# Kernel tuning notes

Measured on AMD Instinct MI355X. Metric: run time of the kernel, lower is better.

The kernel has to match this reference:

```python
import jax, jax.numpy as jnp
import numpy as np


def setup_inputs() -> dict:
    key = jax.random.key(0)
    ks = jax.random.split(key, 8)
    B, L, C = 128, 196, 2048  # batch, locations (att_size^2), channels
    H, D = 512, 1024          # att_hid_size, decoder hidden_size
    return {
        "att_features": jax.random.normal(ks[0], (B, L, C), dtype=jnp.float32),
        "h": jax.random.normal(ks[1], (B, D), dtype=jnp.float32),
        "Wc": jax.random.normal(ks[2], (L, H), dtype=jnp.float32) * 0.05,
        "bc": jax.random.normal(ks[3], (H,), dtype=jnp.float32) * 0.05,
        "Wh": jax.random.normal(ks[4], (D, H), dtype=jnp.float32) * 0.05,
        "bh": jax.random.normal(ks[5], (H,), dtype=jnp.float32) * 0.05,
        "wa": jax.random.normal(ks[6], (H,), dtype=jnp.float32) * 0.05,
        "ba": jnp.zeros((1,), dtype=jnp.float32),
    }


def reference(att_features, h, Wc, bc, Wh, bh, wa, ba):
    B, L, C = att_features.shape
    # reshape to (B, locations, C) then permute -> (B, C, locations)
    x = jnp.transpose(att_features.reshape(B, L, C), (0, 2, 1))  # (B, C, L)
    ca = jnp.einsum('bcl,lh->bch', x, Wc) + bc                   # channel2att: (B, C, H)
    ph = h @ Wh + bh                                              # h2att: (B, H)
    # alpha_net(tanh(broadcast add)) -> (B, C)
    scores = jnp.einsum('bch,h->bc', jnp.tanh(ca + ph[:, None, :]), wa) + ba[0]
    weights = jax.nn.softmax(scores, axis=1)                      # softmax over channels
    # bmm: (B,1,C) @ (B,C,L) -> (B, L)
    weighted = jnp.einsum('bc,bcl->bl', weights, x)
    return weighted, weights
```

## Files before the change

### kernel.cpp

```cpp
#include <hip/hip_runtime.h>

#define B_   128
#define L_   196
#define C_   2048
#define H_   512
#define D_   1024
#define KP   224
#define ALD  232
#define CT   128
#define HM   128
#define NITER 28

typedef __bf16 bf16x8 __attribute__((ext_vector_type(8)));
typedef __bf16 bf16x4 __attribute__((ext_vector_type(4)));
typedef float  f32x4  __attribute__((ext_vector_type(4)));

__global__ __launch_bounds__(256) void k_wc(const float* __restrict__ Wc, __bf16* __restrict__ wcb) {
    int tid = blockIdx.x * 256 + threadIdx.x;
    int hh = tid / KP;
    int k  = tid - hh * KP;
    float v = (k < L_) ? Wc[(size_t)k * H_ + hh] : 0.0f;
    wcb[tid] = (__bf16)v;
}

__global__ __launch_bounds__(512) void k_ph(const float* __restrict__ h, const float* __restrict__ Wh,
                                            const float* __restrict__ bh, const float* __restrict__ bc,
                                            float* __restrict__ ph_ws) {
    int b0 = blockIdx.x * 4;
    int t = threadIdx.x;
    __shared__ float hs[4][D_];
    for (int idx = t; idx < 4 * D_; idx += 512)
        hs[idx >> 10][idx & (D_ - 1)] = h[(size_t)(b0 + (idx >> 10)) * D_ + (idx & (D_ - 1))];
    __syncthreads();
    float base = bh[t] + bc[t];
    float a0 = base, a1 = base, a2 = base, a3 = base;
#pragma unroll 8
    for (int d = 0; d < D_; ++d) {
        float wv = Wh[(size_t)d * H_ + t];
        a0 += hs[0][d] * wv; a1 += hs[1][d] * wv; a2 += hs[2][d] * wv; a3 += hs[3][d] * wv;
    }
    ph_ws[(size_t)(b0 + 0) * H_ + t] = a0;
    ph_ws[(size_t)(b0 + 1) * H_ + t] = a1;
    ph_ws[(size_t)(b0 + 2) * H_ + t] = a2;
    ph_ws[(size_t)(b0 + 3) * H_ + t] = a3;
}

__device__ __forceinline__ float fast_tanh(float x) {
    x = fminf(fmaxf(x, -15.f), 15.f);
    float e = __builtin_amdgcn_exp2f(x * 2.8853900817779268f);
    return 1.0f - 2.0f * __builtin_amdgcn_rcpf(e + 1.0f);
}

__device__ __forceinline__ void stage_wc(const __bf16* __restrict__ wcb, __bf16* dst,
                                         int hc, int kk, int wid, int lane) {
#pragma unroll
    for (int jj = 0; jj < 2; ++jj) {
        int i = wid * 2 + jj;
        const __bf16* g = wcb + (size_t)(hc * HM + i * 16 + (lane >> 2)) * KP + kk * 32 + (lane & 3) * 8;
        __bf16* lp = dst + i * 512;
        __builtin_amdgcn_global_load_lds((__attribute__((address_space(1))) void*)g,
                                         (__attribute__((address_space(3))) void*)lp, 16, 0, 0);
    }
}

__global__ __launch_bounds__(256) void k_scores(const float* __restrict__ att, const __bf16* __restrict__ wcb,
                                                const float* __restrict__ ph_ws, const float* __restrict__ wa,
                                                const float* __restrict__ ba, float* __restrict__ scores) {
    __shared__ __bf16 att_s[CT * ALD];
    __shared__ __bf16 wc_s[2][HM * 32];
    __shared__ float  sred[2][2][4][16];

    const int t = threadIdx.x;
    const int lane = t & 63, wid = t >> 6;
    const int wm = wid >> 1, wn = wid & 1;
    const int ct = blockIdx.x, b = blockIdx.y;

    stage_wc(wcb, &wc_s[0][0], 0, 0, wid, lane);

    {
        const __bf16 z = (__bf16)0.0f;
        bf16x4 z4 = {z, z, z, z};
        for (int idx = t; idx < CT * 7; idx += 256) {
            int c = idx / 7, kq = idx - (idx / 7) * 7;
            *(bf16x4*)&att_s[c * ALD + L_ + kq * 4] = z4;
        }
    }
    {
        const float* abase = att + ((size_t)b * L_) * C_ + ct * CT;
        for (int task = t; task < (CT / 4) * (L_ / 4); task += 256) {
            int cq = task & 31;
            int lq = task >> 5;
            const float* ap = abase + (size_t)(lq * 4) * C_ + cq * 4;
            f32x4 r0 = *(const f32x4*)(ap);
            f32x4 r1 = *(const f32x4*)(ap + C_);
            f32x4 r2 = *(const f32x4*)(ap + 2 * C_);
            f32x4 r3 = *(const f32x4*)(ap + 3 * C_);
#pragma unroll
            for (int i2 = 0; i2 < 4; ++i2) {
                bf16x4 v = {(__bf16)r0[i2], (__bf16)r1[i2], (__bf16)r2[i2], (__bf16)r3[i2]};
                *(bf16x4*)&att_s[(cq * 4 + i2) * ALD + lq * 4] = v;
            }
        }
    }
    __syncthreads();

    const int aoff = (wm * 64 + (lane & 15)) * 32 + (lane >> 4) * 8;
    const int boff = (wn * 64 + (lane & 15)) * ALD + (lane >> 4) * 8;

    f32x4 zero4 = {0.f, 0.f, 0.f, 0.f};
    f32x4 acc[4][4];
#pragma unroll
    for (int mf = 0; mf < 4; ++mf)
#pragma unroll
        for (int nf = 0; nf < 4; ++nf) acc[mf][nf] = zero4;
    float spart[4] = {0.f, 0.f, 0.f, 0.f};

    for (int i = 0; i < NITER; ++i) {
        const int hc = i / 7;
        const int kk = i - hc * 7;
        const int buf = i & 1;
        if (i + 1 < NITER) {
            const int i2 = i + 1;
            stage_wc(wcb, &wc_s[buf ^ 1][0], i2 / 7, i2 - (i2 / 7) * 7, wid, lane);
        }
        bf16x8 afr[4], bfr[4];
#pragma unroll
        for (int mf = 0; mf < 4; ++mf) afr[mf] = *(const bf16x8*)&wc_s[buf][aoff + mf * 512];
#pragma unroll
        for (int nf = 0; nf < 4; ++nf) bfr[nf] = *(const bf16x8*)&att_s[boff + nf * 16 * ALD + kk * 32];
#pragma unroll
        for (int mf = 0; mf < 4; ++mf)
#pragma unroll
            for (int nf = 0; nf < 4; ++nf)
                acc[mf][nf] = __builtin_amdgcn_mfma_f32_16x16x32_bf16(afr[mf], bfr[nf], acc[mf][nf], 0, 0, 0);

        if (kk == 6) {
            const int rbase = hc * HM + wm * 64 + (lane >> 4) * 4;
#pragma unroll
            for (int mf = 0; mf < 4; ++mf) {
                const int row = rbase + mf * 16;
                f32x4 phv = *(const f32x4*)&ph_ws[(size_t)b * H_ + row];
                f32x4 wav = *(const f32x4*)&wa[row];
#pragma unroll
                for (int nf = 0; nf < 4; ++nf) {
                    f32x4 tv = acc[mf][nf];
                    float ssum = 0.f;
#pragma unroll
                    for (int r = 0; r < 4; ++r) {
                        float x = tv[r] + phv[r];
                        ssum += fast_tanh(x) * wav[r];
                    }
                    spart[nf] += ssum;
                    acc[mf][nf] = zero4;
                }
            }
        }
        __syncthreads();
    }

#pragma unroll
    for (int nf = 0; nf < 4; ++nf) {
        spart[nf] += __shfl_xor(spart[nf], 16);
        spart[nf] += __shfl_xor(spart[nf], 32);
    }
    if ((lane >> 4) == 0) {
#pragma unroll
        for (int nf = 0; nf < 4; ++nf) sred[wm][wn][nf][lane] = spart[nf];
    }
    __syncthreads();
    if (wm == 0 && (lane >> 4) == 0) {
        const float ba0 = ba[0];
#pragma unroll
        for (int nf = 0; nf < 4; ++nf) {
            float v = sred[0][wn][nf][lane] + sred[1][wn][nf][lane] + ba0;
            scores[(size_t)b * C_ + ct * CT + wn * 64 + nf * 16 + lane] = v;
        }
    }
}

__global__ __launch_bounds__(256) void k_softmax(const float* __restrict__ sc, float* __restrict__ wout) {
    int b = blockIdx.x, t = threadIdx.x;
    int lane = t & 63, wid = t >> 6;
    const float* sp = sc + (size_t)b * C_;
    float v[8];
#pragma unroll
    for (int j = 0; j < 8; ++j) v[j] = sp[j * 256 + t];
    float m = v[0];
#pragma unroll
    for (int j = 1; j < 8; ++j) m = fmaxf(m, v[j]);
#pragma unroll
    for (int off = 32; off >= 1; off >>= 1) m = fmaxf(m, __shfl_xor(m, off));
    __shared__ float red[4];
    if (lane == 0) red[wid] = m;
    __syncthreads();
    m = fmaxf(fmaxf(red[0], red[1]), fmaxf(red[2], red[3]));
    float s = 0.f;
#pragma unroll
    for (int j = 0; j < 8; ++j) {
        v[j] = __builtin_amdgcn_exp2f((v[j] - m) * 1.4426950408889634f);
        s += v[j];
    }
#pragma unroll
    for (int off = 32; off >= 1; off >>= 1) s += __shfl_xor(s, off);
    __shared__ float red2[4];
    if (lane == 0) red2[wid] = s;
    __syncthreads();
    s = red2[0] + red2[1] + red2[2] + red2[3];
    float inv = __builtin_amdgcn_rcpf(s);
#pragma unroll
    for (int j = 0; j < 8; ++j) wout[(size_t)b * C_ + j * 256 + t] = v[j] * inv;
}

__global__ __launch_bounds__(256) void k_weighted(const float* __restrict__ att, const float* __restrict__ w,
                                                  float* __restrict__ out) {
    int b = blockIdx.y;
    int wid = threadIdx.x >> 6, lane = threadIdx.x & 63;
    int l = blockIdx.x * 4 + wid;
    const float* ap = att + ((size_t)b * L_ + l) * C_;
    const float* wp = w + (size_t)b * C_;
    float acc = 0.f;
#pragma unroll
    for (int j = 0; j < 8; ++j) {
        int c = j * 256 + lane * 4;
        f32x4 a4 = *(const f32x4*)(ap + c);
        f32x4 w4 = *(const f32x4*)(wp + c);
        acc += a4[0] * w4[0] + a4[1] * w4[1] + a4[2] * w4[2] + a4[3] * w4[3];
    }
#pragma unroll
    for (int off = 32; off >= 1; off >>= 1) acc += __shfl_xor(acc, off);
    if (lane == 0) out[(size_t)b * L_ + l] = acc;
}

extern "C" void kernel_launch(void* const* d_in, const int* in_sizes, int n_in,
                              void* d_out, int out_size, void* d_ws, size_t ws_size,
                              hipStream_t stream) {
    const float* att = (const float*)d_in[0];
    const float* h   = (const float*)d_in[1];
    const float* Wc  = (const float*)d_in[2];
    const float* bc  = (const float*)d_in[3];
    const float* Wh  = (const float*)d_in[4];
    const float* bh  = (const float*)d_in[5];
    const float* wa  = (const float*)d_in[6];
    const float* ba  = (const float*)d_in[7];
    float* out = (float*)d_out;

    float* ph_ws  = (float*)d_ws;
    float* scores = ph_ws + B_ * H_;
    __bf16* wcb   = (__bf16*)(scores + (size_t)B_ * C_);

    k_wc      <<<dim3((H_ * KP) / 256), 256, 0, stream>>>(Wc, wcb);
    k_ph      <<<dim3(B_ / 4), 512, 0, stream>>>(h, Wh, bh, bc, ph_ws);
    k_scores  <<<dim3(C_ / CT, B_), 256, 0, stream>>>(att, wcb, ph_ws, wa, ba, scores);
    k_softmax <<<dim3(B_), 256, 0, stream>>>(scores, out + B_ * L_);
    k_weighted<<<dim3(L_ / 4, B_), 256, 0, stream>>>(att, out + B_ * L_, out);
}
```

Measured before the change: 481.8 us.

## Rework scores GEMM tiling with swizzled LDS, register-held Wc, and fuse softmax+weighted

The scores kernel moves to 512-thread blocks covering 256 channels with the whole attention tile staged in a swizzled LDS layout. Staging is now pipelined with the MFMA loop, so the input copy overlaps compute and the per-iteration barriers after staging are dropped. Wc is pre-packed into MFMA fragment order and loaded straight from global memory into registers with prefetch, replacing the LDS double buffer. Softmax and the weighted sum are fused into one kernel that keeps the weights in shared memory. The price is higher register and LDS use per block (128KB dynamic LDS, 32 accumulators per lane), which may limit occupancy, plus softmax being recomputed in 4 blocks per batch.

```diff
diff --git a/kernel.cpp b/kernel.cpp
--- a/kernel.cpp
+++ b/kernel.cpp
@@ -6,21 +6,31 @@
 #define H_   512
 #define D_   1024
 #define KP   224
-#define ALD  232
-#define CT   128
-#define HM   128
-#define NITER 28
+#define CT   256
+#define NITER 14
+
+#define SMEM_BYTES (131072 + 4096)
 
 typedef __bf16 bf16x8 __attribute__((ext_vector_type(8)));
-typedef __bf16 bf16x4 __attribute__((ext_vector_type(4)));
+typedef float  f32x2  __attribute__((ext_vector_type(2)));
 typedef float  f32x4  __attribute__((ext_vector_type(4)));
 
-__global__ __launch_bounds__(256) void k_wc(const float* __restrict__ Wc, __bf16* __restrict__ wcb) {
-    int tid = blockIdx.x * 256 + threadIdx.x;
-    int hh = tid / KP;
-    int k  = tid - hh * KP;
-    float v = (k < L_) ? Wc[(size_t)k * H_ + hh] : 0.0f;
-    wcb[tid] = (__bf16)v;
+__device__ __forceinline__ int permc(int c) { return ((c >> 2) & 7) ^ ((c & 2) << 1); }
+
+__global__ __launch_bounds__(256) void k_wc3(const float* __restrict__ Wc, __bf16* __restrict__ wcb3) {
+    int grp = blockIdx.x * 256 + threadIdx.x;
+    int m  = grp & 15;
+    int g  = (grp >> 4) & 3;
+    int rb = (grp >> 6) & 31;
+    int kk = grp >> 11;
+    int h  = rb * 16 + m;
+    bf16x8 v;
+#pragma unroll
+    for (int j = 0; j < 8; ++j) {
+        int k = kk * 32 + g * 8 + j;
+        v[j] = (k < L_) ? (__bf16)Wc[(size_t)k * H_ + h] : (__bf16)0.0f;
+    }
+    *(bf16x8*)&wcb3[(size_t)grp * 8] = v;
 }
 
 __global__ __launch_bounds__(512) void k_ph(const float* __restrict__ h, const float* __restrict__ Wh,
@@ -51,184 +61,199 @@
     return 1.0f - 2.0f * __builtin_amdgcn_rcpf(e + 1.0f);
 }
 
-__device__ __forceinline__ void stage_wc(const __bf16* __restrict__ wcb, __bf16* dst,
-                                         int hc, int kk, int wid, int lane) {
-#pragma unroll
-    for (int jj = 0; jj < 2; ++jj) {
-        int i = wid * 2 + jj;
-        const __bf16* g = wcb + (size_t)(hc * HM + i * 16 + (lane >> 2)) * KP + kk * 32 + (lane & 3) * 8;
-        __bf16* lp = dst + i * 512;
-        __builtin_amdgcn_global_load_lds((__attribute__((address_space(1))) void*)g,
-                                         (__attribute__((address_space(3))) void*)lp, 16, 0, 0);
-    }
-}
-
-__global__ __launch_bounds__(256) void k_scores(const float* __restrict__ att, const __bf16* __restrict__ wcb,
-                                                const float* __restrict__ ph_ws, const float* __restrict__ wa,
-                                                const float* __restrict__ ba, float* __restrict__ scores) {
-    __shared__ __bf16 att_s[CT * ALD];
-    __shared__ __bf16 wc_s[2][HM * 32];
-    __shared__ float  sred[2][2][4][16];
-
-    const int t = threadIdx.x;
-    const int lane = t & 63, wid = t >> 6;
+__global__ __launch_bounds__(512, 2) void k_scores(const float* __restrict__ att, const __bf16* __restrict__ wcb3,
+                                                   const float* __restrict__ ph_ws, const float* __restrict__ wa,
+                                                   const float* __restrict__ ba, float* __restrict__ scores) {
+    extern __shared__ char smem[];
+    __bf16* att_s = (__bf16*)smem;
+    float*  sred  = (float*)(smem + 131072);
+
+    const int t = threadIdx.x, lane = t & 63, wid = t >> 6;
     const int wm = wid >> 1, wn = wid & 1;
     const int ct = blockIdx.x, b = blockIdx.y;
-
-    stage_wc(wcb, &wc_s[0][0], 0, 0, wid, lane);
-
-    {
-        const __bf16 z = (__bf16)0.0f;
-        bf16x4 z4 = {z, z, z, z};
-        for (int idx = t; idx < CT * 7; idx += 256) {
-            int c = idx / 7, kq = idx - (idx / 7) * 7;
-            *(bf16x4*)&att_s[c * ALD + L_ + kq * 4] = z4;
-        }
-    }
-    {
-        const float* abase = att + ((size_t)b * L_) * C_ + ct * CT;
-        for (int task = t; task < (CT / 4) * (L_ / 4); task += 256) {
-            int cq = task & 31;
-            int lq = task >> 5;
-            const float* ap = abase + (size_t)(lq * 4) * C_ + cq * 4;
-            f32x4 r0 = *(const f32x4*)(ap);
-            f32x4 r1 = *(const f32x4*)(ap + C_);
-            f32x4 r2 = *(const f32x4*)(ap + 2 * C_);
-            f32x4 r3 = *(const f32x4*)(ap + 3 * C_);
-#pragma unroll
-            for (int i2 = 0; i2 < 4; ++i2) {
-                bf16x4 v = {(__bf16)r0[i2], (__bf16)r1[i2], (__bf16)r2[i2], (__bf16)r3[i2]};
-                *(bf16x4*)&att_s[(cq * 4 + i2) * ALD + lq * 4] = v;
-            }
-        }
-    }
-    __syncthreads();
-
-    const int aoff = (wm * 64 + (lane & 15)) * 32 + (lane >> 4) * 8;
-    const int boff = (wn * 64 + (lane & 15)) * ALD + (lane >> 4) * 8;
+    const float* attb = att + ((size_t)b * L_) * C_ + ct * CT;
+
+    const int cpr = t & 127, sl = t >> 7;
+    const int c0s = cpr * 2;
+    const int pmS = permc(c0s);
+
+    const int n_ = lane & 15, g_ = lane >> 4;
+    const int crow0 = wn * 128 + n_;
+    const int t2 = (n_ & 2) << 1;
+    const int qb = crow0 >> 2;
+
+    f32x2 sv[8];
+    auto STAGE_LOAD = [&](int kk) {
+#pragma unroll
+        for (int j = 0; j < 8; ++j) {
+            int l = kk * 32 + sl * 8 + j;
+            if (l < L_) sv[j] = *(const f32x2*)(attb + (size_t)l * C_ + c0s);
+            else { sv[j][0] = 0.f; sv[j][1] = 0.f; }
+        }
+    };
+    auto STAGE_WRITE = [&](int kk) {
+        int p = (kk * 4 + sl) ^ pmS;
+        bf16x8 r0, r1;
+#pragma unroll
+        for (int j = 0; j < 8; ++j) { r0[j] = (__bf16)sv[j][0]; r1[j] = (__bf16)sv[j][1]; }
+        *(bf16x8*)&att_s[c0s * 256 + p * 8] = r0;
+        *(bf16x8*)&att_s[(c0s + 1) * 256 + p * 8] = r1;
+    };
+
+    bf16x8 afr[4], afrN[4];
+    const __bf16* apA = wcb3 + (size_t)lane * 8;
+    auto ALOAD = [&](int it, bf16x8* dst) {
+        int hc = (it >= 7) ? 1 : 0;
+        int kk = it - hc * 7;
+#pragma unroll
+        for (int mf = 0; mf < 4; ++mf) {
+            int rb = hc * 16 + wm * 4 + mf;
+            dst[mf] = *(const bf16x8*)(apA + (size_t)(kk * 32 + rb) * 512);
+        }
+    };
+
+    ALOAD(0, afr);
+    STAGE_LOAD(0);
+    STAGE_WRITE(0);
+    __syncthreads();
 
     f32x4 zero4 = {0.f, 0.f, 0.f, 0.f};
-    f32x4 acc[4][4];
+    f32x4 acc[4][8];
 #pragma unroll
     for (int mf = 0; mf < 4; ++mf)
 #pragma unroll
-        for (int nf = 0; nf < 4; ++nf) acc[mf][nf] = zero4;
-    float spart[4] = {0.f, 0.f, 0.f, 0.f};
-
-    for (int i = 0; i < NITER; ++i) {
-        const int hc = i / 7;
-        const int kk = i - hc * 7;
-        const int buf = i & 1;
-        if (i + 1 < NITER) {
-            const int i2 = i + 1;
-            stage_wc(wcb, &wc_s[buf ^ 1][0], i2 / 7, i2 - (i2 / 7) * 7, wid, lane);
-        }
-        bf16x8 afr[4], bfr[4];
-#pragma unroll
-        for (int mf = 0; mf < 4; ++mf) afr[mf] = *(const bf16x8*)&wc_s[buf][aoff + mf * 512];
-#pragma unroll
-        for (int nf = 0; nf < 4; ++nf) bfr[nf] = *(const bf16x8*)&att_s[boff + nf * 16 * ALD + kk * 32];
+        for (int nf = 0; nf < 8; ++nf) acc[mf][nf] = zero4;
+    float spart[8] = {0.f, 0.f, 0.f, 0.f, 0.f, 0.f, 0.f, 0.f};
+
+    for (int it = 0; it < NITER; ++it) {
+        const int hc = (it >= 7) ? 1 : 0;
+        const int kk = it - hc * 7;
+
+        if (it + 1 < NITER) ALOAD(it + 1, afrN);
+        if (it < 6) STAGE_LOAD(it + 1);
+
+        bf16x8 bfr[8];
+        const int sb = kk * 4 + g_;
+#pragma unroll
+        for (int nf = 0; nf < 8; ++nf) {
+            int p = sb ^ (((qb + nf * 4) & 7) ^ t2);
+            bfr[nf] = *(const bf16x8*)&att_s[(crow0 + nf * 16) * 256 + p * 8];
+        }
 #pragma unroll
         for (int mf = 0; mf < 4; ++mf)
 #pragma unroll
-            for (int nf = 0; nf < 4; ++nf)
+            for (int nf = 0; nf < 8; ++nf)
                 acc[mf][nf] = __builtin_amdgcn_mfma_f32_16x16x32_bf16(afr[mf], bfr[nf], acc[mf][nf], 0, 0, 0);
 
+        if (it < 6) STAGE_WRITE(it + 1);
+
         if (kk == 6) {
-            const int rbase = hc * HM + wm * 64 + (lane >> 4) * 4;
+            const int rbase = hc * 256 + wm * 64 + g_ * 4;
 #pragma unroll
             for (int mf = 0; mf < 4; ++mf) {
                 const int row = rbase + mf * 16;
                 f32x4 phv = *(const f32x4*)&ph_ws[(size_t)b * H_ + row];
                 f32x4 wav = *(const f32x4*)&wa[row];
 #pragma unroll
-                for (int nf = 0; nf < 4; ++nf) {
+                for (int nf = 0; nf < 8; ++nf) {
                     f32x4 tv = acc[mf][nf];
-                    float ssum = 0.f;
-#pragma unroll
-                    for (int r = 0; r < 4; ++r) {
-                        float x = tv[r] + phv[r];
-                        ssum += fast_tanh(x) * wav[r];
-                    }
-                    spart[nf] += ssum;
+                    float ss = 0.f;
+#pragma unroll
+                    for (int r = 0; r < 4; ++r)
+                        ss += fast_tanh(tv[r] + phv[r]) * wav[r];
+                    spart[nf] += ss;
                     acc[mf][nf] = zero4;
                 }
             }
         }
-        __syncthreads();
-    }
-
-#pragma unroll
-    for (int nf = 0; nf < 4; ++nf) {
+
+        if (it < 6) __syncthreads();
+
+        if (it + 1 < NITER) {
+#pragma unroll
+            for (int mf = 0; mf < 4; ++mf) afr[mf] = afrN[mf];
+        }
+    }
+
+#pragma unroll
+    for (int nf = 0; nf < 8; ++nf) {
         spart[nf] += __shfl_xor(spart[nf], 16);
         spart[nf] += __shfl_xor(spart[nf], 32);
     }
-    if ((lane >> 4) == 0) {
-#pragma unroll
-        for (int nf = 0; nf < 4; ++nf) sred[wm][wn][nf][lane] = spart[nf];
-    }
-    __syncthreads();
-    if (wm == 0 && (lane >> 4) == 0) {
+    if (g_ == 0) {
+#pragma unroll
+        for (int nf = 0; nf < 8; ++nf) sred[(wid * 8 + nf) * 16 + n_] = spart[nf];
+    }
+    __syncthreads();
+    if (wid < 2 && g_ == 0) {
         const float ba0 = ba[0];
 #pragma unroll
-        for (int nf = 0; nf < 4; ++nf) {
-            float v = sred[0][wn][nf][lane] + sred[1][wn][nf][lane] + ba0;
-            scores[(size_t)b * C_ + ct * CT + wn * 64 + nf * 16 + lane] = v;
-        }
-    }
-}
-
-__global__ __launch_bounds__(256) void k_softmax(const float* __restrict__ sc, float* __restrict__ wout) {
-    int b = blockIdx.x, t = threadIdx.x;
-    int lane = t & 63, wid = t >> 6;
+        for (int nf = 0; nf < 8; ++nf) {
+            float v = ba0;
+#pragma unroll
+            for (int wmm = 0; wmm < 4; ++wmm) v += sred[((wmm * 2 + wid) * 8 + nf) * 16 + n_];
+            scores[(size_t)b * C_ + ct * CT + wid * 128 + nf * 16 + n_] = v;
+        }
+    }
+}
+
+__global__ __launch_bounds__(512) void k_fused(const float* __restrict__ att, const float* __restrict__ sc,
+                                               float* __restrict__ out) {
+    __shared__ float w_s[C_];
+    __shared__ float red[8], red2[8];
+    const int b = blockIdx.y, q = blockIdx.x;
+    const int t = threadIdx.x;
+    const int lane = t & 63, wid = t >> 6;
+
     const float* sp = sc + (size_t)b * C_;
-    float v[8];
-#pragma unroll
-    for (int j = 0; j < 8; ++j) v[j] = sp[j * 256 + t];
-    float m = v[0];
-#pragma unroll
-    for (int j = 1; j < 8; ++j) m = fmaxf(m, v[j]);
+    float v[4];
+#pragma unroll
+    for (int j = 0; j < 4; ++j) v[j] = sp[j * 512 + t];
+    float m = fmaxf(fmaxf(v[0], v[1]), fmaxf(v[2], v[3]));
 #pragma unroll
     for (int off = 32; off >= 1; off >>= 1) m = fmaxf(m, __shfl_xor(m, off));
-    __shared__ float red[4];
     if (lane == 0) red[wid] = m;
     __syncthreads();
-    m = fmaxf(fmaxf(red[0], red[1]), fmaxf(red[2], red[3]));
+#pragma unroll
+    for (int w = 0; w < 8; ++w) m = fmaxf(m, red[w]);
     float s = 0.f;
 #pragma unroll
-    for (int j = 0; j < 8; ++j) {
+    for (int j = 0; j < 4; ++j) {
         v[j] = __builtin_amdgcn_exp2f((v[j] - m) * 1.4426950408889634f);
         s += v[j];
     }
 #pragma unroll
     for (int off = 32; off >= 1; off >>= 1) s += __shfl_xor(s, off);
-    __shared__ float red2[4];
     if (lane == 0) red2[wid] = s;
     __syncthreads();
-    s = red2[0] + red2[1] + red2[2] + red2[3];
-    float inv = __builtin_amdgcn_rcpf(s);
-#pragma unroll
-    for (int j = 0; j < 8; ++j) wout[(size_t)b * C_ + j * 256 + t] = v[j] * inv;
-}
-
-__global__ __launch_bounds__(256) void k_weighted(const float* __restrict__ att, const float* __restrict__ w,
-                                                  float* __restrict__ out) {
-    int b = blockIdx.y;
-    int wid = threadIdx.x >> 6, lane = threadIdx.x & 63;
-    int l = blockIdx.x * 4 + wid;
-    const float* ap = att + ((size_t)b * L_ + l) * C_;
-    const float* wp = w + (size_t)b * C_;
-    float acc = 0.f;
-#pragma unroll
-    for (int j = 0; j < 8; ++j) {
-        int c = j * 256 + lane * 4;
-        f32x4 a4 = *(const f32x4*)(ap + c);
-        f32x4 w4 = *(const f32x4*)(wp + c);
-        acc += a4[0] * w4[0] + a4[1] * w4[1] + a4[2] * w4[2] + a4[3] * w4[3];
-    }
-#pragma unroll
-    for (int off = 32; off >= 1; off >>= 1) acc += __shfl_xor(acc, off);
-    if (lane == 0) out[(size_t)b * L_ + l] = acc;
+    s = 0.f;
+#pragma unroll
+    for (int w = 0; w < 8; ++w) s += red2[w];
+    float inv = 1.0f / s;
+    float* wout = out + B_ * L_;
+#pragma unroll
+    for (int j = 0; j < 4; ++j) {
+        float wv = v[j] * inv;
+        w_s[j * 512 + t] = wv;
+        if (q == 0) wout[(size_t)b * C_ + j * 512 + t] = wv;
+    }
+    __syncthreads();
+
+    for (int l = wid; l < 49; l += 8) {
+        int gl = q * 49 + l;
+        const float* ap = att + ((size_t)b * L_ + gl) * C_;
+        float acc = 0.f;
+#pragma unroll
+        for (int j = 0; j < 8; ++j) {
+            int c = j * 256 + lane * 4;
+            f32x4 a4 = *(const f32x4*)(ap + c);
+            f32x4 w4 = *(const f32x4*)&w_s[c];
+            acc += a4[0] * w4[0] + a4[1] * w4[1] + a4[2] * w4[2] + a4[3] * w4[3];
+        }
+#pragma unroll
+        for (int off = 32; off >= 1; off >>= 1) acc += __shfl_xor(acc, off);
+        if (lane == 0) out[(size_t)b * L_ + gl] = acc;
+    }
 }
 
 extern "C" void kernel_launch(void* const* d_in, const int* in_sizes, int n_in,
@@ -246,11 +271,12 @@
 
     float* ph_ws  = (float*)d_ws;
     float* scores = ph_ws + B_ * H_;
-    __bf16* wcb   = (__bf16*)(scores + (size_t)B_ * C_);
-
-    k_wc      <<<dim3((H_ * KP) / 256), 256, 0, stream>>>(Wc, wcb);
-    k_ph      <<<dim3(B_ / 4), 512, 0, stream>>>(h, Wh, bh, bc, ph_ws);
-    k_scores  <<<dim3(C_ / CT, B_), 256, 0, stream>>>(att, wcb, ph_ws, wa, ba, scores);
-    k_softmax <<<dim3(B_), 256, 0, stream>>>(scores, out + B_ * L_);
-    k_weighted<<<dim3(L_ / 4, B_), 256, 0, stream>>>(att, out + B_ * L_, out);
-}
+    __bf16* wcb3  = (__bf16*)(scores + (size_t)B_ * C_);
+
+    hipFuncSetAttribute((const void*)k_scores, hipFuncAttributeMaxDynamicSharedMemorySize, SMEM_BYTES);
+
+    k_wc3   <<<dim3(56), 256, 0, stream>>>(Wc, wcb3);
+    k_ph    <<<dim3(B_ / 4), 512, 0, stream>>>(h, Wh, bh, bc, ph_ws);
+    k_scores<<<dim3(C_ / CT, B_), 512, SMEM_BYTES, stream>>>(att, wcb3, ph_ws, wa, ba, scores);
+    k_fused <<<dim3(4, B_), 512, 0, stream>>>(att, scores, out);
+}
```

After: 454.8 us. -5.6%, faster.
